# Kernel tuning notes

Measured on AMD Instinct MI355X. Metric: run time of the kernel, lower is better.

## Reference

```python
import jax, jax.numpy as jnp
import numpy as np

WINDOW = 128
STRIDE = 16

def setup_inputs() -> dict:
    key = jax.random.key(0)
    input_data = jax.random.normal(key, (16, 4096, 128), dtype=jnp.float32)
    return {"input_data": input_data}

def reference(input_data) -> jnp.ndarray:
    B, T, F = input_data.shape
    num_windows = (T - WINDOW) // STRIDE + 1  # 249
    # time indices for every window: [num_windows, WINDOW]
    idx = jnp.arange(num_windows)[:, None] * STRIDE + jnp.arange(WINDOW)[None, :]
    # gather overlapping windows: [B, num_windows, WINDOW, F]
    windows = input_data[:, idx, :]
    # per-window X^T X / WINDOW: [B, num_windows, F, F]
    pccs = jnp.einsum('bwlf,bwlg->bwfg', windows, windows) / WINDOW
    return pccs
```

## Files before the change

### kernel.cpp

```cpp
#include <hip/hip_runtime.h>

#define WINDOW 128
#define STRIDE 16
#define NWIN   249
#define NF     128
#define SEQ    4096
#define LROWS  160

typedef _Float16 f16;
typedef _Float16 f16x2 __attribute__((ext_vector_type(2)));
typedef _Float16 f16x8 __attribute__((ext_vector_type(8)));
typedef float    f32x4 __attribute__((ext_vector_type(4)));

union V8 { f16x8 v8; f16x2 v2[4]; };

__device__ __forceinline__ void stage8(const float* __restrict__ src, f16* lds,
                                       int f0, int l0) {
    f32x4 rows[8];
    #pragma unroll
    for (int j = 0; j < 8; ++j)
        rows[j] = *(const f32x4*)&src[(size_t)(l0 + j) * NF + f0];
    const int cbase = l0 >> 3;
    #pragma unroll
    for (int d = 0; d < 4; ++d) {
        const int f = f0 + d;
        V8 u;
        #pragma unroll
        for (int jj = 0; jj < 4; ++jj) {
            auto p = __builtin_amdgcn_cvt_pkrtz(rows[2 * jj][d], rows[2 * jj + 1][d]);
            u.v2[jj] = *(f16x2*)&p;
        }
        u.v8 = u.v8 * (f16)0.08838834764831845f;
        const int ch = (l0 < 128) ? (cbase ^ (f & 15))
                                  : (16 + ((cbase & 3) ^ (f & 3)));
        *(f16x8*)&lds[f * LROWS + ch * 8] = u.v8;
    }
}

template<int CO>
__device__ __forceinline__ void compute_and_store(const f16* lds, int c, int q,
                                                  int wid, float* __restrict__ dst) {
    f32x4 acc[2][8];
    #pragma unroll
    for (int i = 0; i < 2; ++i)
        #pragma unroll
        for (int t = 0; t < 8; ++t)
            acc[i][t] = f32x4{0.f, 0.f, 0.f, 0.f};

    #pragma unroll
    for (int ks = 0; ks < 4; ++ks) {
        const int clog = CO + 4 * ks + q;
        int pc;
        if (CO == 0) pc = clog ^ c;
        else pc = (clog < 16) ? (clog ^ c) : (16 + ((clog & 3) ^ (c & 3)));
        const int off = pc * 8;

        f16x8 bfrag[8];
        #pragma unroll
        for (int t = 0; t < 8; ++t)
            bfrag[t] = *(const f16x8*)&lds[(16 * t + c) * LROWS + off];
        const f16x8 a0 = *(const f16x8*)&lds[(16 * (2 * wid + 0) + c) * LROWS + off];
        const f16x8 a1 = *(const f16x8*)&lds[(16 * (2 * wid + 1) + c) * LROWS + off];
        #pragma unroll
        for (int t = 0; t < 8; ++t) {
            acc[0][t] = __builtin_amdgcn_mfma_f32_16x16x32_f16(a0, bfrag[t], acc[0][t], 0, 0, 0);
            acc[1][t] = __builtin_amdgcn_mfma_f32_16x16x32_f16(a1, bfrag[t], acc[1][t], 0, 0, 0);
        }
    }

    #pragma unroll
    for (int i = 0; i < 2; ++i) {
        const int rowbase = 16 * (2 * wid + i) + 4 * q;
        #pragma unroll
        for (int t = 0; t < 8; ++t)
            #pragma unroll
            for (int r = 0; r < 4; ++r)
                dst[(rowbase + r) * NF + 16 * t + c] = acc[i][t][r];
    }
}

__global__ __launch_bounds__(256) void pcc_kernel(const float* __restrict__ in,
                                                  float* __restrict__ out) {
    __shared__ f16 lds[NF * LROWS];

    const int tid = threadIdx.x;
    const int wp  = blockIdx.x;
    const int b   = blockIdx.y;
    const bool full = (wp < 124);
    const int stage_base = full ? 32 * wp : (SEQ - 144);

    const float* src = in + ((size_t)b * SEQ + stage_base) * NF;
    const int f0 = 4 * (tid & 31);
    const int lh = tid >> 5;

    stage8(src, lds, f0, 8 * lh);
    stage8(src, lds, f0, 64 + 8 * lh);
    if (tid < 64)
        stage8(src, lds, f0, 128 + 8 * lh);
    __syncthreads();

    const int lane = tid & 63;
    const int wid  = tid >> 6;
    const int q    = lane >> 4;
    const int c    = lane & 15;

    float* outb = out + (size_t)b * NWIN * (NF * NF);
    if (full)
        compute_and_store<0>(lds, c, q, wid, outb + (size_t)(2 * wp) * (NF * NF));
    const int w1 = full ? (2 * wp + 1) : (NWIN - 1);
    compute_and_store<2>(lds, c, q, wid, outb + (size_t)w1 * (NF * NF));
}

extern "C" void kernel_launch(void* const* d_in, const int* in_sizes, int n_in,
                              void* d_out, int out_size, void* d_ws, size_t ws_size,
                              hipStream_t stream) {
    (void)in_sizes; (void)n_in; (void)d_ws; (void)ws_size; (void)out_size;
    const float* in = (const float*)d_in[0];
    float* out = (float*)d_out;
    dim3 grid(125, 16);
    pcc_kernel<<<grid, dim3(256, 1, 1), 0, stream>>>(in, out);
}
```

Measured before the change: 295.4 us.

## Switch to 32x32x16 MFMA tiles with nontemporal stores and block swizzle

Replaces the 16x16x32 MFMA tiling (each wave owning 32 rows by 128 columns) with 32x32x16 MFMA tiles arranged as a 2x2 wave grid of 64x64 blocks. This cuts the number of LDS fragment loads per MFMA. Output stores become nontemporal to avoid polluting cache with the large write-only result. Block indices are swizzled across XCDs, and launch bounds request 4 blocks per CU. The cost is a different LDS access pattern, which may add bank conflicts, and store coalescing changes.

```diff
diff --git a/kernel.cpp b/kernel.cpp
--- a/kernel.cpp
+++ b/kernel.cpp
@@ -11,6 +11,7 @@
 typedef _Float16 f16x2 __attribute__((ext_vector_type(2)));
 typedef _Float16 f16x8 __attribute__((ext_vector_type(8)));
 typedef float    f32x4 __attribute__((ext_vector_type(4)));
+typedef float    f32x16 __attribute__((ext_vector_type(16)));
 
 union V8 { f16x8 v8; f16x2 v2[4]; };
 
@@ -38,54 +39,69 @@
 }
 
 template<int CO>
-__device__ __forceinline__ void compute_and_store(const f16* lds, int c, int q,
-                                                  int wid, float* __restrict__ dst) {
-    f32x4 acc[2][8];
+__device__ __forceinline__ void compute_and_store(const f16* lds, int lane,
+                                                  int wr, int wc, float* __restrict__ dst) {
+    const int c15 = lane & 15;
+    const int c31 = lane & 31;
+    const int h   = lane >> 5;
+
+    f32x16 acc[2][2];
     #pragma unroll
     for (int i = 0; i < 2; ++i)
         #pragma unroll
-        for (int t = 0; t < 8; ++t)
-            acc[i][t] = f32x4{0.f, 0.f, 0.f, 0.f};
+        for (int j = 0; j < 2; ++j)
+            acc[i][j] = (f32x16)(0.0f);
 
     #pragma unroll
-    for (int ks = 0; ks < 4; ++ks) {
-        const int clog = CO + 4 * ks + q;
+    for (int ks = 0; ks < 8; ++ks) {
+        const int clog = CO + 2 * ks + h;
         int pc;
-        if (CO == 0) pc = clog ^ c;
-        else pc = (clog < 16) ? (clog ^ c) : (16 + ((clog & 3) ^ (c & 3)));
+        if (CO == 0 || CO + 2 * ks + 1 < 16)
+            pc = clog ^ c15;
+        else
+            pc = 16 + ((clog & 3) ^ (lane & 3));
         const int off = pc * 8;
 
-        f16x8 bfrag[8];
+        f16x8 af[2], bf[2];
         #pragma unroll
-        for (int t = 0; t < 8; ++t)
-            bfrag[t] = *(const f16x8*)&lds[(16 * t + c) * LROWS + off];
-        const f16x8 a0 = *(const f16x8*)&lds[(16 * (2 * wid + 0) + c) * LROWS + off];
-        const f16x8 a1 = *(const f16x8*)&lds[(16 * (2 * wid + 1) + c) * LROWS + off];
+        for (int i = 0; i < 2; ++i)
+            af[i] = *(const f16x8*)&lds[(64 * wr + 32 * i + c31) * LROWS + off];
         #pragma unroll
-        for (int t = 0; t < 8; ++t) {
-            acc[0][t] = __builtin_amdgcn_mfma_f32_16x16x32_f16(a0, bfrag[t], acc[0][t], 0, 0, 0);
-            acc[1][t] = __builtin_amdgcn_mfma_f32_16x16x32_f16(a1, bfrag[t], acc[1][t], 0, 0, 0);
-        }
+        for (int j = 0; j < 2; ++j)
+            bf[j] = *(const f16x8*)&lds[(64 * wc + 32 * j + c31) * LROWS + off];
+
+        #pragma unroll
+        for (int i = 0; i < 2; ++i)
+            #pragma unroll
+            for (int j = 0; j < 2; ++j)
+                acc[i][j] = __builtin_amdgcn_mfma_f32_32x32x16_f16(af[i], bf[j], acc[i][j], 0, 0, 0);
     }
 
     #pragma unroll
     for (int i = 0; i < 2; ++i) {
-        const int rowbase = 16 * (2 * wid + i) + 4 * q;
+        const int R0 = 64 * wr + 32 * i + 4 * h;
         #pragma unroll
-        for (int t = 0; t < 8; ++t)
+        for (int j = 0; j < 2; ++j) {
+            float* dcol = dst + 64 * wc + 32 * j + c31;
             #pragma unroll
-            for (int r = 0; r < 4; ++r)
-                dst[(rowbase + r) * NF + 16 * t + c] = acc[i][t][r];
+            for (int reg = 0; reg < 16; ++reg) {
+                const int row = R0 + (reg & 3) + 8 * (reg >> 2);
+                __builtin_nontemporal_store(acc[i][j][reg], &dcol[(size_t)row * NF]);
+            }
+        }
     }
 }
 
-__global__ __launch_bounds__(256) void pcc_kernel(const float* __restrict__ in,
-                                                  float* __restrict__ out) {
+__global__ __launch_bounds__(256, 4) void pcc_kernel(const float* __restrict__ in,
+                                                     float* __restrict__ out) {
     __shared__ f16 lds[NF * LROWS];
 
+    const int lin = blockIdx.x + 125 * blockIdx.y;
+    const int swz = (lin & 7) * 250 + (lin >> 3);
+    const int wp  = swz % 125;
+    const int b   = swz / 125;
+
     const int tid = threadIdx.x;
-    const int wp  = blockIdx.x;
-    const int b   = blockIdx.y;
     const bool full = (wp < 124);
     const int stage_base = full ? 32 * wp : (SEQ - 144);
 
@@ -101,14 +117,14 @@
 
     const int lane = tid & 63;
     const int wid  = tid >> 6;
-    const int q    = lane >> 4;
-    const int c    = lane & 15;
+    const int wr   = wid >> 1;
+    const int wc   = wid & 1;
 
     float* outb = out + (size_t)b * NWIN * (NF * NF);
     if (full)
-        compute_and_store<0>(lds, c, q, wid, outb + (size_t)(2 * wp) * (NF * NF));
+        compute_and_store<0>(lds, lane, wr, wc, outb + (size_t)(2 * wp) * (NF * NF));
     const int w1 = full ? (2 * wp + 1) : (NWIN - 1);
-    compute_and_store<2>(lds, c, q, wid, outb + (size_t)w1 * (NF * NF));
+    compute_and_store<2>(lds, lane, wr, wc, outb + (size_t)w1 * (NF * NF));
 }
 
 extern "C" void kernel_launch(void* const* d_in, const int* in_sizes, int n_in,
```

Result: no change. 296.7 us (+0.5%).
